# Optimization experiments

Measured on AMD Instinct MI355X. Metric: run time of the kernel, lower is better.

Reference implementation:

```python
import jax, jax.numpy as jnp
import numpy as np

N = 100000   # nodes (single node type 'A')
C = 256      # hidden_channels
OUT = 128    # out_channels
E_RAND = 300000  # random edges; total E = N + E_RAND = 400000
LN_EPS = 1e-5


def _linear_params(key, in_c, out_c):
    kw, kb = jax.random.split(key)
    bound = 1.0 / np.sqrt(in_c)
    W = jax.random.uniform(kw, (out_c, in_c), minval=-bound, maxval=bound, dtype=jnp.float32)
    b = jax.random.uniform(kb, (out_c,), minval=-bound, maxval=bound, dtype=jnp.float32)
    return W, b


def _edges(key):
    # guarantee every node appears in both rows -> unique()/remap in the torch
    # code is the identity, so the subgraph equals the full graph
    k0, k1 = jax.random.split(key)
    base = jnp.arange(N, dtype=jnp.int64)
    row0 = jnp.concatenate([base, jax.random.randint(k0, (E_RAND,), 0, N, dtype=jnp.int64)])
    row1 = jnp.concatenate([base, jax.random.randint(k1, (E_RAND,), 0, N, dtype=jnp.int64)])
    return jnp.stack([row0, row1])


def setup_inputs() -> dict:
    key = jax.random.key(0)
    ks = jax.random.split(key, 12)
    x = jax.random.normal(ks[0], (N, C), dtype=jnp.float32)
    edge_index_r0 = _edges(ks[1])
    edge_index_r1 = _edges(ks[2])
    wl0, bl0 = _linear_params(ks[3], C, C)
    w00, b00 = _linear_params(ks[4], C, C)
    w10, b10 = _linear_params(ks[5], C, C)
    wl1, bl1 = _linear_params(ks[6], C, C)
    w01, b01 = _linear_params(ks[7], C, C)
    w11, b11 = _linear_params(ks[8], C, C)
    Wout, bout = _linear_params(ks[9], C, OUT)
    return dict(
        x=x, edge_index_r0=edge_index_r0, edge_index_r1=edge_index_r1,
        wl0=wl0, bl0=bl0, w00=w00, b00=b00, w10=w10, b10=b10,
        gate0=jnp.float32(0.5), lns0=jnp.ones((C,), jnp.float32), lnb0=jnp.zeros((C,), jnp.float32),
        wl1=wl1, bl1=bl1, w01=w01, b01=b01, w11=w11, b11=b11,
        gate1=jnp.float32(0.5), lns1=jnp.ones((C,), jnp.float32), lnb1=jnp.zeros((C,), jnp.float32),
        Wout=Wout, bout=bout,
    )


def _metapath_layer(x0, h, ei, wl, bl, w0, b0, w1, b1, gate, lns, lnb):
    n = h.shape[0]
    src, dst = ei[0], ei[1]
    # PyG flow='target_to_source', aggr='add': message x_j = h[edge_index[1]],
    # scatter-added at edge_index[0]
    agg = jax.ops.segment_sum(h[dst], src, num_segments=n)
    # original code normalizes by bincount of edge_index[1] (kept faithfully)
    deg = jax.ops.segment_sum(jnp.ones_like(dst, dtype=h.dtype), dst, num_segments=n)
    agg = agg / jnp.clip(deg, 1.0)[:, None]
    g = jax.nn.sigmoid(gate)
    out = (agg @ wl.T + bl) + (1.0 - g) * (h @ w0.T + b0) + g * (x0 @ w1.T + b1)
    out = jax.nn.relu(out)
    mu = out.mean(-1, keepdims=True)
    var = out.var(-1, keepdims=True)
    out = (out - mu) / jnp.sqrt(var + LN_EPS) * lns + lnb
    return out  # dropout is identity in eval mode


def reference(x, edge_index_r0, edge_index_r1,
              wl0, bl0, w00, b00, w10, b10, gate0, lns0, lnb0,
              wl1, bl1, w01, b01, w11, b11, gate1, lns1, lnb1,
              Wout, bout):
    x0 = jax.lax.stop_gradient(x)  # x0_dict is detached in the torch code
    h = x
    # metapath is processed in reverse: conv index 1 first, then conv index 0
    h = _metapath_layer(x0, h, edge_index_r1, wl1, bl1, w01, b01, w11, b11, gate1, lns1, lnb1)
    h = _metapath_layer(x0, h, edge_index_r0, wl0, bl0, w00, b00, w10, b10, gate0, lns0, lnb0)
    return h @ Wout.T + bout
```

## Files before the change

kernel.cpp:

```cpp
#include <hip/hip_runtime.h>

typedef unsigned short u16;
typedef unsigned int   u32;

typedef __attribute__((ext_vector_type(8))) __bf16 bf16x8;
typedef __attribute__((ext_vector_type(8))) unsigned short u16x8;
typedef __attribute__((ext_vector_type(4))) float  f32x4;

#define C      256
#define OUTC   128
#define LN_EPS 1e-5f

__device__ __forceinline__ float bf2f(u16 u) {
    u32 i = ((u32)u) << 16; float f; __builtin_memcpy(&f, &i, 4); return f;
}
__device__ __forceinline__ u16 f2bf(float f) {
    u32 i; __builtin_memcpy(&i, &f, 4);
    u32 r = (i + 0x7FFFu + ((i >> 16) & 1u)) >> 16;
    return (u16)r;
}
__device__ __forceinline__ void load_lds16(const void* g, void* l) {
    __builtin_amdgcn_global_load_lds((const __attribute__((address_space(1))) u32*)g,
                                     (__attribute__((address_space(3))) u32*)l, 16, 0, 0);
}
__device__ __forceinline__ int swz(int row) { return (row + (row >> 2)) & 3; }

#define PREP_BLK 1408
__global__ void prep_combo(const float* wl0, const float* w00, const float* w10,
                           const float* bl0, const float* b00, const float* b10,
                           const float* gate0,
                           const float* wl1, const float* w01, const float* w11,
                           const float* bl1, const float* b01, const float* b11,
                           const float* gate1,
                           const float* Wout, const float* x,
                           u16* __restrict__ WcatA, u16* __restrict__ WcatB,
                           u16* __restrict__ Woutb, float* __restrict__ bcat,
                           u16* __restrict__ xb, size_t n8)
{
    if (blockIdx.x >= PREP_BLK) {
        size_t i = ((size_t)(blockIdx.x - PREP_BLK) * 256 + threadIdx.x);
        if (i >= n8) return;
        const float* p = x + i * 8;
        float4 v0 = *(const float4*)p;
        float4 v1 = *(const float4*)(p + 4);
        u16x8 o;
        o[0] = f2bf(v0.x); o[1] = f2bf(v0.y); o[2] = f2bf(v0.z); o[3] = f2bf(v0.w);
        o[4] = f2bf(v1.x); o[5] = f2bf(v1.y); o[6] = f2bf(v1.z); o[7] = f2bf(v1.w);
        *(u16x8*)(xb + i * 8) = o;
        return;
    }
    int idx = blockIdx.x * 256 + threadIdx.x;
    float gA = 1.f / (1.f + expf(-gate1[0]));
    float gB = 1.f / (1.f + expf(-gate0[0]));
    if (idx < 256 * 512) {
        int n = idx >> 9, k = idx & 511;
        float v;
        if (k < 256) v = wl1[n * 256 + k];
        else         v = (1.f - gA) * w01[n * 256 + (k - 256)] + gA * w11[n * 256 + (k - 256)];
        WcatA[idx] = f2bf(v);
    } else if (idx < 256 * 512 + 256 * 768) {
        int j = idx - 256 * 512;
        int n = j / 768, k = j - n * 768;
        float v;
        if (k < 256)      v = wl0[n * 256 + k];
        else if (k < 512) v = (1.f - gB) * w00[n * 256 + (k - 256)];
        else              v = gB * w10[n * 256 + (k - 512)];
        WcatB[j] = f2bf(v);
    } else {
        int j = idx - (256 * 512 + 256 * 768);
        if (j < OUTC * C) Woutb[j] = f2bf(Wout[j]);
    }
    if (idx < 512) {
        int nn = idx & 255;
        if (idx < 256) bcat[idx] = bl1[nn] + (1.f - gA) * b01[nn] + gA * b11[nn];
        else           bcat[idx] = bl0[nn] + (1.f - gB) * b00[nn] + gB * b10[nn];
    }
}

__global__ void count_edges2(const int* __restrict__ ei1, const int* __restrict__ ei0,
                             int* __restrict__ cnt1, int* __restrict__ deg1,
                             int* __restrict__ cnt0, int* __restrict__ deg0,
                             int E, int Nn, int ebg)
{
    int b = blockIdx.x;
    const int* ei; int *cnt, *deg;
    if (b < ebg) { ei = ei1; cnt = cnt1; deg = deg1; }
    else         { b -= ebg; ei = ei0; cnt = cnt0; deg = deg0; }
    int idx = b * 256 + threadIdx.x;
    if (idx >= E) return;
    int s = ei[idx], d = ei[E + idx];
    if ((unsigned)s >= (unsigned)Nn || (unsigned)d >= (unsigned)Nn) return;
    atomicAdd(cnt + s, 1);
    atomicAdd(deg + d, 1);
}

__global__ void block_sums2(const int* __restrict__ cnt1, const int* __restrict__ cnt0,
                            int* __restrict__ parts1, int* __restrict__ parts0,
                            int n, int nblk)
{
    int b = blockIdx.x;
    const int* counts; int* partials;
    if (b < nblk) { counts = cnt1; partials = parts1; }
    else          { b -= nblk; counts = cnt0; partials = parts0; }
    int i = b * 256 + threadIdx.x;
    int v = (i < n) ? counts[i] : 0;
    #pragma unroll
    for (int off = 32; off; off >>= 1) v += __shfl_down(v, off, 64);
    __shared__ int ws[4];
    if ((threadIdx.x & 63) == 0) ws[threadIdx.x >> 6] = v;
    __syncthreads();
    if (threadIdx.x == 0) partials[b] = ws[0] + ws[1] + ws[2] + ws[3];
}

__global__ void scan_partials2(int* __restrict__ parts1, int* __restrict__ parts0, int nblk)
{
    int* partials = blockIdx.x ? parts0 : parts1;
    __shared__ int buf[1024];
    int tid = threadIdx.x;
    int v = (tid < nblk) ? partials[tid] : 0;
    buf[tid] = v; __syncthreads();
    for (int off = 1; off < 1024; off <<= 1) {
        int t = (tid >= off) ? buf[tid - off] : 0;
        __syncthreads();
        buf[tid] += t;
        __syncthreads();
    }
    if (tid < nblk) partials[tid] = buf[tid] - v;
}

__global__ void make_offsets2(int* __restrict__ cnt1, int* __restrict__ cnt0,
                              const int* __restrict__ parts1, const int* __restrict__ parts0,
                              int* __restrict__ off1a, int* __restrict__ off0a,
                              int n, int nblk)
{
    int b = blockIdx.x;
    int* counts_cursor; const int* partials; int* offsets;
    if (b < nblk) { counts_cursor = cnt1; partials = parts1; offsets = off1a; }
    else          { b -= nblk; counts_cursor = cnt0; partials = parts0; offsets = off0a; }
    __shared__ int buf[256];
    int i = b * 256 + threadIdx.x;
    int cnt = (i < n) ? counts_cursor[i] : 0;
    buf[threadIdx.x] = cnt; __syncthreads();
    for (int off = 1; off < 256; off <<= 1) {
        int t = (threadIdx.x >= off) ? buf[threadIdx.x - off] : 0;
        __syncthreads();
        buf[threadIdx.x] += t;
        __syncthreads();
    }
    int off = partials[b] + buf[threadIdx.x] - cnt;
    if (i < n) {
        offsets[i] = off;
        counts_cursor[i] = off;
        if (i == n - 1) offsets[n] = off + cnt;
    }
}

__global__ void fill_edges2(const int* __restrict__ ei1, const int* __restrict__ ei0,
                            int* __restrict__ cur1, int* __restrict__ cur0,
                            int* __restrict__ ed1, int* __restrict__ ed0,
                            int E, int Nn, int ebg)
{
    int b = blockIdx.x;
    const int* ei; int *cursor, *edgedst;
    if (b < ebg) { ei = ei1; cursor = cur1; edgedst = ed1; }
    else         { b -= ebg; ei = ei0; cursor = cur0; edgedst = ed0; }
    int idx = b * 256 + threadIdx.x;
    if (idx >= E) return;
    int s = ei[idx], d = ei[E + idx];
    if ((unsigned)s >= (unsigned)Nn || (unsigned)d >= (unsigned)Nn) return;
    int p = atomicAdd(cursor + s, 1);
    edgedst[p] = d;
}

__global__ __launch_bounds__(256) void gather_kernel(
    const int* __restrict__ offsets, const int* __restrict__ edgedst,
    const int* __restrict__ degcnt, const u16* __restrict__ h,
    u16* __restrict__ aggb, int Nn)
{
    int node = blockIdx.x * 4 + (threadIdx.x >> 6);
    if (node >= Nn) return;
    int lane = threadIdx.x & 63;
    int beg = offsets[node], end = offsets[node + 1];
    float4 a0 = {0.f, 0.f, 0.f, 0.f}, a1 = {0.f, 0.f, 0.f, 0.f};
    int e = beg;
    for (; e + 1 < end; e += 2) {
        int d0 = edgedst[e], d1 = edgedst[e + 1];
        ushort4 v0 = *(const ushort4*)(h + (size_t)d0 * C + lane * 4);
        ushort4 v1 = *(const ushort4*)(h + (size_t)d1 * C + lane * 4);
        a0.x += bf2f(v0.x); a0.y += bf2f(v0.y); a0.z += bf2f(v0.z); a0.w += bf2f(v0.w);
        a1.x += bf2f(v1.x); a1.y += bf2f(v1.y); a1.z += bf2f(v1.z); a1.w += bf2f(v1.w);
    }
    if (e < end) {
        int d0 = edgedst[e];
        ushort4 v0 = *(const ushort4*)(h + (size_t)d0 * C + lane * 4);
        a0.x += bf2f(v0.x); a0.y += bf2f(v0.y); a0.z += bf2f(v0.z); a0.w += bf2f(v0.w);
    }
    float inv = 1.0f / fmaxf((float)degcnt[node], 1.0f);
    ushort4 o;
    o.x = f2bf((a0.x + a1.x) * inv); o.y = f2bf((a0.y + a1.y) * inv);
    o.z = f2bf((a0.z + a1.z) * inv); o.w = f2bf((a0.w + a1.w) * inv);
    *(ushort4*)(aggb + (size_t)node * C + lane * 4) = o;
}

template <int NSEG>
__global__ __launch_bounds__(512, 4) void layer_gemm(
    const u16* __restrict__ s0, const u16* __restrict__ s1, const u16* __restrict__ s2,
    const u16* __restrict__ W,
    const float* __restrict__ bcat,
    const float* __restrict__ lns, const float* __restrict__ lnb,
    u16* __restrict__ Hout, int Nnodes)
{
    constexpr int WK = NSEG * 256;
    constexpr int KT = NSEG * 8;

    __shared__ u16 Alds[2][128 * 32];
    __shared__ u16 Blds[2][256 * 32];
    __shared__ float lnpart[128][4][2];

    const int tid  = threadIdx.x;
    const int wave = tid >> 6, lane = tid & 63;
    const int wave_m = wave & 1, wave_n = wave >> 1;
    const int q = lane >> 4, l15 = lane & 15;
    const int m0 = blockIdx.x * 128;

    const int srow = (wave << 4) + (lane >> 2);
    int anode = m0 + srow; if (anode >= Nnodes) anode = Nnodes - 1;
    const int asc = (lane & 3) ^ swz(srow);
    const size_t a_goff = (size_t)anode * C + asc * 8;
    const int a_lo = wave << 9;

    const u16* bgp[2]; int b_lo[2];
    #pragma unroll
    for (int i = 0; i < 2; ++i) {
        int cb = wave + i * 8;
        int brow = (cb << 4) + (lane >> 2);
        int bsc = (lane & 3) ^ swz(brow);
        bgp[i]  = W + brow * WK + bsc * 8;
        b_lo[i] = cb << 9;
    }

    int aoff[4], boff[4];
    #pragma unroll
    for (int t = 0; t < 4; ++t) {
        int ar = wave_m * 64 + t * 16 + l15;
        aoff[t] = ar * 32 + ((q ^ swz(ar)) << 3);
        int br = wave_n * 64 + t * 16 + l15;
        boff[t] = br * 32 + ((q ^ swz(br)) << 3);
    }

    f32x4 acc[4][4] = {};

    auto stage = [&](int b, int kt) {
        const u16* Asrc = (kt < 8) ? s0 : ((NSEG == 2 || kt < 16) ? s1 : s2);
        load_lds16(Asrc + a_goff + ((kt & 7) << 5), &Alds[b][a_lo]);
        int k0 = kt << 5;
        load_lds16(bgp[0] + k0, &Blds[b][b_lo[0]]);
        load_lds16(bgp[1] + k0, &Blds[b][b_lo[1]]);
    };
    auto compute = [&](const u16* __restrict__ Ab, const u16* __restrict__ Bb) {
        bf16x8 af[4], bfr[4];
        #pragma unroll
        for (int t = 0; t < 4; ++t) af[t]  = *(const bf16x8*)(Ab + aoff[t]);
        #pragma unroll
        for (int f = 0; f < 4; ++f) bfr[f] = *(const bf16x8*)(Bb + boff[f]);
        #pragma unroll
        for (int t = 0; t < 4; ++t)
            #pragma unroll
            for (int f = 0; f < 4; ++f)
                acc[t][f] = __builtin_amdgcn_mfma_f32_16x16x32_bf16(af[t], bfr[f], acc[t][f], 0, 0, 0);
    };

    stage(0, 0);
    stage(1, 1);
    for (int kt = 0; kt < KT - 2; kt += 2) {
        asm volatile("s_waitcnt vmcnt(3)" ::: "memory");
        __builtin_amdgcn_s_barrier();
        __builtin_amdgcn_sched_barrier(0);
        compute(&Alds[0][0], &Blds[0][0]);
        __builtin_amdgcn_sched_barrier(0);
        __builtin_amdgcn_s_barrier();
        stage(0, kt + 2);
        asm volatile("s_waitcnt vmcnt(3)" ::: "memory");
        __builtin_amdgcn_s_barrier();
        __builtin_amdgcn_sched_barrier(0);
        compute(&Alds[1][0], &Blds[1][0]);
        __builtin_amdgcn_sched_barrier(0);
        __builtin_amdgcn_s_barrier();
        stage(1, kt + 3);
    }
    asm volatile("s_waitcnt vmcnt(3)" ::: "memory");
    __builtin_amdgcn_s_barrier();
    __builtin_amdgcn_sched_barrier(0);
    compute(&Alds[0][0], &Blds[0][0]);
    asm volatile("s_waitcnt vmcnt(0)" ::: "memory");
    __builtin_amdgcn_s_barrier();
    __builtin_amdgcn_sched_barrier(0);
    compute(&Alds[1][0], &Blds[1][0]);

    float bias[4], lsc[4], lbi[4];
    #pragma unroll
    for (int f = 0; f < 4; ++f) {
        int n = wave_n * 64 + f * 16 + l15;
        bias[f] = bcat[n]; lsc[f] = lns[n]; lbi[f] = lnb[n];
    }
    #pragma unroll
    for (int t = 0; t < 4; ++t)
        #pragma unroll
        for (int r = 0; r < 4; ++r) {
            float p = 0.f, pp = 0.f;
            #pragma unroll
            for (int f = 0; f < 4; ++f) {
                float v = acc[t][f][r] + bias[f];
                v = fmaxf(v, 0.f);
                acc[t][f][r] = v;
                p += v; pp += v * v;
            }
            #pragma unroll
            for (int off = 1; off < 16; off <<= 1) {
                p  += __shfl_xor(p,  off, 16);
                pp += __shfl_xor(pp, off, 16);
            }
            if (l15 == 0) {
                int row = wave_m * 64 + t * 16 + q * 4 + r;
                lnpart[row][wave_n][0] = p;
                lnpart[row][wave_n][1] = pp;
            }
        }
    __syncthreads();
    #pragma unroll
    for (int t = 0; t < 4; ++t)
        #pragma unroll
        for (int r = 0; r < 4; ++r) {
            int row = wave_m * 64 + t * 16 + q * 4 + r;
            int node = m0 + row;
            if (node < Nnodes) {
                float S1 = lnpart[row][0][0] + lnpart[row][1][0]
                         + lnpart[row][2][0] + lnpart[row][3][0];
                float S2 = lnpart[row][0][1] + lnpart[row][1][1]
                         + lnpart[row][2][1] + lnpart[row][3][1];
                float mean = S1 * (1.f / 256.f);
                float var  = fmaxf(S2 * (1.f / 256.f) - mean * mean, 0.f);
                float rstd = rsqrtf(var + LN_EPS);
                u16* op = Hout + (size_t)node * C;
                #pragma unroll
                for (int f = 0; f < 4; ++f) {
                    int n = wave_n * 64 + f * 16 + l15;
                    op[n] = f2bf((acc[t][f][r] - mean) * rstd * lsc[f] + lbi[f]);
                }
            }
        }
}

__global__ __launch_bounds__(512, 4) void final_gemm(
    const u16* __restrict__ A, const u16* __restrict__ W,
    const float* __restrict__ bout, float* __restrict__ out, int Nnodes)
{
    __shared__ u16 Alds[2][128 * 32];
    __shared__ u16 Blds[2][128 * 32];

    const int tid = threadIdx.x;
    const int wave = tid >> 6, lane = tid & 63;
    const int wave_m = wave & 1, wave_n = wave >> 1;
    const int q = lane >> 4, l15 = lane & 15;
    const int m0 = blockIdx.x * 128;

    const int srow = (wave << 4) + (lane >> 2);
    int anode = m0 + srow; if (anode >= Nnodes) anode = Nnodes - 1;
    const int asc = (lane & 3) ^ swz(srow);
    const size_t a_goff = (size_t)anode * C + asc * 8;
    const int a_lo = wave << 9;

    const int bsc = (lane & 3) ^ swz(srow);
    const u16* bgp = W + srow * C + bsc * 8;
    const int b_lo = wave << 9;

    int aoff[4], boff[2];
    #pragma unroll
    for (int t = 0; t < 4; ++t) {
        int ar = wave_m * 64 + t * 16 + l15;
        aoff[t] = ar * 32 + ((q ^ swz(ar)) << 3);
    }
    #pragma unroll
    for (int f = 0; f < 2; ++f) {
        int br = wave_n * 32 + f * 16 + l15;
        boff[f] = br * 32 + ((q ^ swz(br)) << 3);
    }

    f32x4 acc[4][2] = {};

    auto stage = [&](int b, int kt) {
        int k0 = kt << 5;
        load_lds16(A + a_goff + k0, &Alds[b][a_lo]);
        load_lds16(bgp + k0, &Blds[b][b_lo]);
    };
    auto compute = [&](const u16* __restrict__ Ab, const u16* __restrict__ Bb) {
        bf16x8 af[4], bfr[2];
        #pragma unroll
        for (int t = 0; t < 4; ++t) af[t]  = *(const bf16x8*)(Ab + aoff[t]);
        #pragma unroll
        for (int f = 0; f < 2; ++f) bfr[f] = *(const bf16x8*)(Bb + boff[f]);
        #pragma unroll
        for (int t = 0; t < 4; ++t)
            #pragma unroll
            for (int f = 0; f < 2; ++f)
                acc[t][f] = __builtin_amdgcn_mfma_f32_16x16x32_bf16(af[t], bfr[f], acc[t][f], 0, 0, 0);
    };

    stage(0, 0);
    stage(1, 1);
    for (int kt = 0; kt < 6; kt += 2) {
        asm volatile("s_waitcnt vmcnt(2)" ::: "memory");
        __builtin_amdgcn_s_barrier();
        __builtin_amdgcn_sched_barrier(0);
        compute(&Alds[0][0], &Blds[0][0]);
        __builtin_amdgcn_sched_barrier(0);
        __builtin_amdgcn_s_barrier();
        stage(0, kt + 2);
        asm volatile("s_waitcnt vmcnt(2)" ::: "memory");
        __builtin_amdgcn_s_barrier();
        __builtin_amdgcn_sched_barrier(0);
        compute(&Alds[1][0], &Blds[1][0]);
        __builtin_amdgcn_sched_barrier(0);
        __builtin_amdgcn_s_barrier();
        stage(1, kt + 3);
    }
    asm volatile("s_waitcnt vmcnt(2)" ::: "memory");
    __builtin_amdgcn_s_barrier();
    __builtin_amdgcn_sched_barrier(0);
    compute(&Alds[0][0], &Blds[0][0]);
    asm volatile("s_waitcnt vmcnt(0)" ::: "memory");
    __builtin_amdgcn_s_barrier();
    __builtin_amdgcn_sched_barrier(0);
    compute(&Alds[1][0], &Blds[1][0]);

    float bias[2];
    #pragma unroll
    for (int f = 0; f < 2; ++f) bias[f] = bout[wave_n * 32 + f * 16 + l15];
    #pragma unroll
    for (int t = 0; t < 4; ++t)
        #pragma unroll
        for (int r = 0; r < 4; ++r) {
            int row = wave_m * 64 + t * 16 + q * 4 + r;
            int node = m0 + row;
            if (node < Nnodes) {
                float* op = out + (size_t)node * OUTC;
                #pragma unroll
                for (int f = 0; f < 2; ++f) {
                    int n = wave_n * 32 + f * 16 + l15;
                    op[n] = acc[t][f][r] + bias[f];
                }
            }
        }
}

extern "C" void kernel_launch(void* const* d_in, const int* in_sizes, int n_in,
                              void* d_out, int out_size, void* d_ws, size_t ws_size,
                              hipStream_t stream)
{
    const float* x    = (const float*)d_in[0];
    const int*   ei0  = (const int*)d_in[1];
    const int*   ei1  = (const int*)d_in[2];
    const float* wl0  = (const float*)d_in[3];
    const float* bl0  = (const float*)d_in[4];
    const float* w00  = (const float*)d_in[5];
    const float* b00  = (const float*)d_in[6];
    const float* w10  = (const float*)d_in[7];
    const float* b10  = (const float*)d_in[8];
    const float* gate0= (const float*)d_in[9];
    const float* lns0 = (const float*)d_in[10];
    const float* lnb0 = (const float*)d_in[11];
    const float* wl1  = (const float*)d_in[12];
    const float* bl1  = (const float*)d_in[13];
    const float* w01  = (const float*)d_in[14];
    const float* b01  = (const float*)d_in[15];
    const float* w11  = (const float*)d_in[16];
    const float* b11  = (const float*)d_in[17];
    const float* gate1= (const float*)d_in[18];
    const float* lns1 = (const float*)d_in[19];
    const float* lnb1 = (const float*)d_in[20];
    const float* Wout = (const float*)d_in[21];
    const float* bout = (const float*)d_in[22];

    const int N = in_sizes[0] / C;
    const int E = in_sizes[1] / 2;

    char* w = (char*)d_ws;
    u16*   WcatA = (u16*)w;   w += (size_t)256 * 512 * 2;
    u16*   WcatB = (u16*)w;   w += (size_t)256 * 768 * 2;
    u16*   Woutb = (u16*)w;   w += (size_t)OUTC * C * 2;
    float* bcat  = (float*)w; w += 4096;
    int*   cnt1  = (int*)w;   w += (size_t)N * 4;
    int*   deg1  = (int*)w;   w += (size_t)N * 4;
    int*   cnt0  = (int*)w;   w += (size_t)N * 4;
    int*   deg0  = (int*)w;   w += (size_t)N * 4;
    int*   off1  = (int*)w;   w += (((size_t)(N + 1) * 4) + 255) & ~255ull;
    int*   off0  = (int*)w;   w += (((size_t)(N + 1) * 4) + 255) & ~255ull;
    int*   parts1= (int*)w;   w += 4096;
    int*   parts0= (int*)w;   w += 4096;
    int*   ed1   = (int*)w;   w += (size_t)E * 4;
    int*   ed0   = (int*)w;   w += (size_t)E * 4;
    u16*   xb    = (u16*)w;   w += (size_t)N * C * 2;
    u16*   aggb  = (u16*)w;   w += (size_t)N * C * 2;
    u16*   h1    = (u16*)w;   w += (size_t)N * C * 2;

    const int eb_grid = (E + 255) / 256;
    const int nblk    = (N + 255) / 256;
    const int gt_grid = (N + 3) / 4;
    const int gm_grid = (N + 127) / 128;
    const size_t n8   = (size_t)N * C / 8;
    const int xc_blk  = (int)((n8 + 255) / 256);
    u16* h2 = (u16*)d_out;

    hipMemsetAsync(cnt1, 0, (size_t)4 * N * 4, stream);
    prep_combo<<<PREP_BLK + xc_blk, 256, 0, stream>>>(
        wl0, w00, w10, bl0, b00, b10, gate0,
        wl1, w01, w11, bl1, b01, b11, gate1,
        Wout, x, WcatA, WcatB, Woutb, bcat, xb, n8);

    count_edges2 <<<2 * eb_grid, 256, 0, stream>>>(ei1, ei0, cnt1, deg1, cnt0, deg0, E, N, eb_grid);
    block_sums2  <<<2 * nblk, 256, 0, stream>>>(cnt1, cnt0, parts1, parts0, N, nblk);
    scan_partials2<<<2, 1024, 0, stream>>>(parts1, parts0, nblk);
    make_offsets2<<<2 * nblk, 256, 0, stream>>>(cnt1, cnt0, parts1, parts0, off1, off0, N, nblk);
    fill_edges2  <<<2 * eb_grid, 256, 0, stream>>>(ei1, ei0, cnt1, cnt0, ed1, ed0, E, N, eb_grid);

    gather_kernel<<<gt_grid, 256, 0, stream>>>(off1, ed1, deg1, xb, aggb, N);
    layer_gemm<2><<<gm_grid, 512, 0, stream>>>(aggb, xb, nullptr, WcatA, bcat,
                                               lns1, lnb1, h1, N);

    gather_kernel<<<gt_grid, 256, 0, stream>>>(off0, ed0, deg0, h1, aggb, N);
    layer_gemm<3><<<gm_grid, 512, 0, stream>>>(aggb, h1, xb, WcatB, bcat + C,
                                               lns0, lnb0, h2, N);

    final_gemm<<<gm_grid, 512, 0, stream>>>(h2, Woutb, bout, (float*)d_out, N);
}
```

Baseline: 536.6 us.

## Widen layer GEMM to 256-row tiles with K=64 stages and vectorize gather

The layer GEMM now processes 256 node rows per block instead of 128. It stages 64-wide K slices in two halves using a new swizzled LDS layout held in 136 KB of dynamic shared memory, and interleaves MFMA issue with LDS reads and prefetches under s_setprio. The aim is to double reuse of the concatenated weight tile per block and to hide more global-load latency. The cost is a larger accumulator array, a launch-bounds minimum of 2 blocks instead of 4, and heavy LDS use that limits occupancy. The gather kernel also changes: each half-wave reads 16-byte bf16 vectors for a different edge, and the two halves are combined with a lane shuffle, which means fewer, wider loads per edge row.

```diff
diff --git a/kernel.cpp b/kernel.cpp
--- a/kernel.cpp
+++ b/kernel.cpp
@@ -180,30 +180,45 @@
     int node = blockIdx.x * 4 + (threadIdx.x >> 6);
     if (node >= Nn) return;
     int lane = threadIdx.x & 63;
+    int half = lane >> 5, l5 = lane & 31;
     int beg = offsets[node], end = offsets[node + 1];
-    float4 a0 = {0.f, 0.f, 0.f, 0.f}, a1 = {0.f, 0.f, 0.f, 0.f};
-    int e = beg;
-    for (; e + 1 < end; e += 2) {
-        int d0 = edgedst[e], d1 = edgedst[e + 1];
-        ushort4 v0 = *(const ushort4*)(h + (size_t)d0 * C + lane * 4);
-        ushort4 v1 = *(const ushort4*)(h + (size_t)d1 * C + lane * 4);
-        a0.x += bf2f(v0.x); a0.y += bf2f(v0.y); a0.z += bf2f(v0.z); a0.w += bf2f(v0.w);
-        a1.x += bf2f(v1.x); a1.y += bf2f(v1.y); a1.z += bf2f(v1.z); a1.w += bf2f(v1.w);
-    }
-    if (e < end) {
-        int d0 = edgedst[e];
-        ushort4 v0 = *(const ushort4*)(h + (size_t)d0 * C + lane * 4);
-        a0.x += bf2f(v0.x); a0.y += bf2f(v0.y); a0.z += bf2f(v0.z); a0.w += bf2f(v0.w);
+    float a0[8] = {}, a1[8] = {};
+    int p = beg;
+    for (; p + 3 < end; p += 4) {
+        int d0 = edgedst[p + half];
+        int d1 = edgedst[p + 2 + half];
+        u16x8 v0 = *(const u16x8*)(h + (size_t)d0 * C + l5 * 8);
+        u16x8 v1 = *(const u16x8*)(h + (size_t)d1 * C + l5 * 8);
+        #pragma unroll
+        for (int j = 0; j < 8; ++j) { a0[j] += bf2f(v0[j]); a1[j] += bf2f(v1[j]); }
+    }
+    if (p + 1 < end) {
+        int d0 = edgedst[p + half];
+        u16x8 v0 = *(const u16x8*)(h + (size_t)d0 * C + l5 * 8);
+        #pragma unroll
+        for (int j = 0; j < 8; ++j) a0[j] += bf2f(v0[j]);
+        p += 2;
+    }
+    if (p < end && half == 0) {
+        int d0 = edgedst[p];
+        u16x8 v0 = *(const u16x8*)(h + (size_t)d0 * C + l5 * 8);
+        #pragma unroll
+        for (int j = 0; j < 8; ++j) a1[j] += bf2f(v0[j]);
     }
     float inv = 1.0f / fmaxf((float)degcnt[node], 1.0f);
-    ushort4 o;
-    o.x = f2bf((a0.x + a1.x) * inv); o.y = f2bf((a0.y + a1.y) * inv);
-    o.z = f2bf((a0.z + a1.z) * inv); o.w = f2bf((a0.w + a1.w) * inv);
-    *(ushort4*)(aggb + (size_t)node * C + lane * 4) = o;
+    u16x8 o;
+    #pragma unroll
+    for (int j = 0; j < 8; ++j) {
+        float s = a0[j] + a1[j];
+        s += __shfl_xor(s, 32);
+        o[j] = f2bf(s * inv);
+    }
+    if (half == 0)
+        *(u16x8*)(aggb + (size_t)node * C + l5 * 8) = o;
 }
 
 template <int NSEG>
-__global__ __launch_bounds__(512, 4) void layer_gemm(
+__global__ __launch_bounds__(512, 2) void layer_gemm8(
     const u16* __restrict__ s0, const u16* __restrict__ s1, const u16* __restrict__ s2,
     const u16* __restrict__ W,
     const float* __restrict__ bcat,
@@ -211,91 +226,148 @@
     u16* __restrict__ Hout, int Nnodes)
 {
     constexpr int WK = NSEG * 256;
-    constexpr int KT = NSEG * 8;
-
-    __shared__ u16 Alds[2][128 * 32];
-    __shared__ u16 Blds[2][256 * 32];
-    __shared__ float lnpart[128][4][2];
+    constexpr int T  = NSEG * 4;
+
+    extern __shared__ char smem[];
+    u16*   A_e    = (u16*)smem;
+    u16*   B_e    = (u16*)(smem + 65536);
+    float* lnpart = (float*)(smem + 131072);
 
     const int tid  = threadIdx.x;
     const int wave = tid >> 6, lane = tid & 63;
     const int wave_m = wave & 1, wave_n = wave >> 1;
     const int q = lane >> 4, l15 = lane & 15;
-    const int m0 = blockIdx.x * 128;
-
-    const int srow = (wave << 4) + (lane >> 2);
-    int anode = m0 + srow; if (anode >= Nnodes) anode = Nnodes - 1;
-    const int asc = (lane & 3) ^ swz(srow);
-    const size_t a_goff = (size_t)anode * C + asc * 8;
-    const int a_lo = wave << 9;
-
-    const u16* bgp[2]; int b_lo[2];
+    const int m0 = blockIdx.x * 256;
+
+    size_t a_goff[2], b_goff[2];
+    int ldso[2];
     #pragma unroll
     for (int i = 0; i < 2; ++i) {
-        int cb = wave + i * 8;
-        int brow = (cb << 4) + (lane >> 2);
-        int bsc = (lane & 3) ^ swz(brow);
-        bgp[i]  = W + brow * WK + bsc * 8;
-        b_lo[i] = cb << 9;
-    }
-
-    int aoff[4], boff[4];
-    #pragma unroll
-    for (int t = 0; t < 4; ++t) {
-        int ar = wave_m * 64 + t * 16 + l15;
-        aoff[t] = ar * 32 + ((q ^ swz(ar)) << 3);
-        int br = wave_n * 64 + t * 16 + l15;
-        boff[t] = br * 32 + ((q ^ swz(br)) << 3);
-    }
-
-    f32x4 acc[4][4] = {};
-
-    auto stage = [&](int b, int kt) {
-        const u16* Asrc = (kt < 8) ? s0 : ((NSEG == 2 || kt < 16) ? s1 : s2);
-        load_lds16(Asrc + a_goff + ((kt & 7) << 5), &Alds[b][a_lo]);
-        int k0 = kt << 5;
-        load_lds16(bgp[0] + k0, &Blds[b][b_lo[0]]);
-        load_lds16(bgp[1] + k0, &Blds[b][b_lo[1]]);
+        int o = i * 8192 + wave * 1024 + lane * 16;
+        int g = o >> 7, slot = (o >> 4) & 7;
+        int bc = slot ^ (g & 7);
+        int r = 2 * g + (bc >> 2), c = bc & 3;
+        int node = m0 + r; if (node >= Nnodes) node = Nnodes - 1;
+        a_goff[i] = (size_t)node * C + c * 8;
+        b_goff[i] = (size_t)r * WK + c * 8;
+        ldso[i]   = i * 8192 + wave * 1024;
+    }
+
+    int aoffE[8], boffE[4];
+    #pragma unroll
+    for (int j = 0; j < 8; ++j) {
+        int r = wave_m * 128 + j * 16 + l15;
+        aoffE[j] = (r >> 1) * 64 + (((((r & 1) << 2) | q) ^ ((r >> 1) & 7)) << 3);
+    }
+    #pragma unroll
+    for (int f = 0; f < 4; ++f) {
+        int r = wave_n * 64 + f * 16 + l15;
+        boffE[f] = (r >> 1) * 64 + (((((r & 1) << 2) | q) ^ ((r >> 1) & 7)) << 3);
+    }
+
+    f32x4 acc[8][4] = {};
+
+    auto stA = [&](int buf, int kh, int t) {
+        const u16* sp = (t < 4) ? s0 : ((NSEG == 2 || t < 8) ? s1 : s2);
+        const u16* base = sp + ((t & 3) << 6) + (kh << 5);
+        #pragma unroll
+        for (int i = 0; i < 2; ++i)
+            load_lds16(base + a_goff[i], (char*)A_e + buf * 32768 + kh * 16384 + ldso[i]);
     };
-    auto compute = [&](const u16* __restrict__ Ab, const u16* __restrict__ Bb) {
+    auto stB = [&](int buf, int kh, int t) {
+        const u16* base = W + (t << 6) + (kh << 5);
+        #pragma unroll
+        for (int i = 0; i < 2; ++i)
+            load_lds16(base + b_goff[i], (char*)B_e + buf * 32768 + kh * 16384 + ldso[i]);
+    };
+
+#define LDA(DST, BASE, MH) \
+    _Pragma("unroll") for (int j = 0; j < 4; ++j) \
+        DST[j] = *(const bf16x8*)((BASE) + aoffE[(MH) * 4 + j]);
+#define LDB(DST, BASE) \
+    _Pragma("unroll") for (int f = 0; f < 4; ++f) \
+        DST[f] = *(const bf16x8*)((BASE) + boffE[f]);
+#define MFMA16(MH, AF, BF) \
+    _Pragma("unroll") for (int j = 0; j < 4; ++j) \
+        _Pragma("unroll") for (int f = 0; f < 4; ++f) \
+            acc[(MH) * 4 + j][f] = __builtin_amdgcn_mfma_f32_16x16x32_bf16( \
+                AF[j], BF[f], acc[(MH) * 4 + j][f], 0, 0, 0);
+#define SBAR()  asm volatile("s_barrier" ::: "memory")
+
+    stA(0, 0, 0); stB(0, 0, 0); stA(0, 1, 0); stB(0, 1, 0);
+
+    int cur = 0;
+    for (int t = 0; t < T - 1; ++t, cur ^= 1) {
+        const u16* Ac = A_e + cur * 16384;
+        const u16* Bc = B_e + cur * 16384;
+        const int nxt = cur ^ 1;
         bf16x8 af[4], bfr[4];
-        #pragma unroll
-        for (int t = 0; t < 4; ++t) af[t]  = *(const bf16x8*)(Ab + aoff[t]);
-        #pragma unroll
-        for (int f = 0; f < 4; ++f) bfr[f] = *(const bf16x8*)(Bb + boff[f]);
-        #pragma unroll
-        for (int t = 0; t < 4; ++t)
-            #pragma unroll
-            for (int f = 0; f < 4; ++f)
-                acc[t][f] = __builtin_amdgcn_mfma_f32_16x16x32_bf16(af[t], bfr[f], acc[t][f], 0, 0, 0);
-    };
-
-    stage(0, 0);
-    stage(1, 1);
-    for (int kt = 0; kt < KT - 2; kt += 2) {
-        asm volatile("s_waitcnt vmcnt(3)" ::: "memory");
-        __builtin_amdgcn_s_barrier();
-        __builtin_amdgcn_sched_barrier(0);
-        compute(&Alds[0][0], &Blds[0][0]);
-        __builtin_amdgcn_sched_barrier(0);
-        __builtin_amdgcn_s_barrier();
-        stage(0, kt + 2);
-        asm volatile("s_waitcnt vmcnt(3)" ::: "memory");
-        __builtin_amdgcn_s_barrier();
-        __builtin_amdgcn_sched_barrier(0);
-        compute(&Alds[1][0], &Blds[1][0]);
-        __builtin_amdgcn_sched_barrier(0);
-        __builtin_amdgcn_s_barrier();
-        stage(1, kt + 3);
-    }
-    asm volatile("s_waitcnt vmcnt(3)" ::: "memory");
-    __builtin_amdgcn_s_barrier();
-    __builtin_amdgcn_sched_barrier(0);
-    compute(&Alds[0][0], &Blds[0][0]);
-    asm volatile("s_waitcnt vmcnt(0)" ::: "memory");
-    __builtin_amdgcn_s_barrier();
-    __builtin_amdgcn_sched_barrier(0);
-    compute(&Alds[1][0], &Blds[1][0]);
+        stA(nxt, 0, t + 1);
+        asm volatile("s_waitcnt vmcnt(6)" ::: "memory");
+        SBAR();
+        __builtin_amdgcn_sched_barrier(0);
+        LDB(bfr, Bc); LDA(af, Ac, 0);
+        __builtin_amdgcn_s_setprio(1);
+        MFMA16(0, af, bfr);
+        __builtin_amdgcn_s_setprio(0);
+        SBAR();
+        LDA(af, Ac, 1);
+        stB(nxt, 0, t + 1);
+        SBAR();
+        __builtin_amdgcn_s_setprio(1);
+        MFMA16(1, af, bfr);
+        __builtin_amdgcn_s_setprio(0);
+        SBAR();
+        stA(nxt, 1, t + 1);
+        asm volatile("s_waitcnt vmcnt(6)" ::: "memory");
+        SBAR();
+        __builtin_amdgcn_sched_barrier(0);
+        LDB(bfr, Bc + 8192); LDA(af, Ac + 8192, 0);
+        __builtin_amdgcn_s_setprio(1);
+        MFMA16(0, af, bfr);
+        __builtin_amdgcn_s_setprio(0);
+        SBAR();
+        LDA(af, Ac + 8192, 1);
+        stB(nxt, 1, t + 1);
+        SBAR();
+        __builtin_amdgcn_s_setprio(1);
+        MFMA16(1, af, bfr);
+        __builtin_amdgcn_s_setprio(0);
+        SBAR();
+    }
+    {
+        const u16* Ac = A_e + cur * 16384;
+        const u16* Bc = B_e + cur * 16384;
+        bf16x8 af[4], bfr[4];
+        asm volatile("s_waitcnt vmcnt(4)" ::: "memory");
+        SBAR();
+        __builtin_amdgcn_sched_barrier(0);
+        LDB(bfr, Bc); LDA(af, Ac, 0);
+        __builtin_amdgcn_s_setprio(1);
+        MFMA16(0, af, bfr);
+        __builtin_amdgcn_s_setprio(0);
+        SBAR();
+        LDA(af, Ac, 1);
+        SBAR();
+        __builtin_amdgcn_s_setprio(1);
+        MFMA16(1, af, bfr);
+        __builtin_amdgcn_s_setprio(0);
+        SBAR();
+        asm volatile("s_waitcnt vmcnt(0)" ::: "memory");
+        SBAR();
+        __builtin_amdgcn_sched_barrier(0);
+        LDB(bfr, Bc + 8192); LDA(af, Ac + 8192, 0);
+        __builtin_amdgcn_s_setprio(1);
+        MFMA16(0, af, bfr);
+        __builtin_amdgcn_s_setprio(0);
+        SBAR();
+        LDA(af, Ac + 8192, 1);
+        SBAR();
+        __builtin_amdgcn_s_setprio(1);
+        MFMA16(1, af, bfr);
+        __builtin_amdgcn_s_setprio(0);
+        SBAR();
+    }
 
     float bias[4], lsc[4], lbi[4];
     #pragma unroll
@@ -304,15 +376,15 @@
         bias[f] = bcat[n]; lsc[f] = lns[n]; lbi[f] = lnb[n];
     }
     #pragma unroll
-    for (int t = 0; t < 4; ++t)
+    for (int t8 = 0; t8 < 8; ++t8)
         #pragma unroll
         for (int r = 0; r < 4; ++r) {
             float p = 0.f, pp = 0.f;
             #pragma unroll
             for (int f = 0; f < 4; ++f) {
-                float v = acc[t][f][r] + bias[f];
+                float v = acc[t8][f][r] + bias[f];
                 v = fmaxf(v, 0.f);
-                acc[t][f][r] = v;
+                acc[t8][f][r] = v;
                 p += v; pp += v * v;
             }
             #pragma unroll
@@ -321,23 +393,23 @@
                 pp += __shfl_xor(pp, off, 16);
             }
             if (l15 == 0) {
-                int row = wave_m * 64 + t * 16 + q * 4 + r;
-                lnpart[row][wave_n][0] = p;
-                lnpart[row][wave_n][1] = pp;
+                int row = wave_m * 128 + t8 * 16 + q * 4 + r;
+                lnpart[row * 8 + wave_n * 2 + 0] = p;
+                lnpart[row * 8 + wave_n * 2 + 1] = pp;
             }
         }
     __syncthreads();
     #pragma unroll
-    for (int t = 0; t < 4; ++t)
+    for (int t8 = 0; t8 < 8; ++t8)
         #pragma unroll
         for (int r = 0; r < 4; ++r) {
-            int row = wave_m * 64 + t * 16 + q * 4 + r;
+            int row = wave_m * 128 + t8 * 16 + q * 4 + r;
             int node = m0 + row;
             if (node < Nnodes) {
-                float S1 = lnpart[row][0][0] + lnpart[row][1][0]
-                         + lnpart[row][2][0] + lnpart[row][3][0];
-                float S2 = lnpart[row][0][1] + lnpart[row][1][1]
-                         + lnpart[row][2][1] + lnpart[row][3][1];
+                float S1 = lnpart[row * 8 + 0] + lnpart[row * 8 + 2]
+                         + lnpart[row * 8 + 4] + lnpart[row * 8 + 6];
+                float S2 = lnpart[row * 8 + 1] + lnpart[row * 8 + 3]
+                         + lnpart[row * 8 + 5] + lnpart[row * 8 + 7];
                 float mean = S1 * (1.f / 256.f);
                 float var  = fmaxf(S2 * (1.f / 256.f) - mean * mean, 0.f);
                 float rstd = rsqrtf(var + LN_EPS);
@@ -345,10 +417,14 @@
                 #pragma unroll
                 for (int f = 0; f < 4; ++f) {
                     int n = wave_n * 64 + f * 16 + l15;
-                    op[n] = f2bf((acc[t][f][r] - mean) * rstd * lsc[f] + lbi[f]);
+                    op[n] = f2bf((acc[t8][f][r] - mean) * rstd * lsc[f] + lbi[f]);
                 }
             }
         }
+#undef LDA
+#undef LDB
+#undef MFMA16
+#undef SBAR
 }
 
 __global__ __launch_bounds__(512, 4) void final_gemm(
@@ -507,8 +583,10 @@
     const int nblk    = (N + 255) / 256;
     const int gt_grid = (N + 3) / 4;
     const int gm_grid = (N + 127) / 128;
+    const int gm8     = (N + 255) / 256;
     const size_t n8   = (size_t)N * C / 8;
     const int xc_blk  = (int)((n8 + 255) / 256);
+    const size_t lds8 = 139264;
     u16* h2 = (u16*)d_out;
 
     hipMemsetAsync(cnt1, 0, (size_t)4 * N * 4, stream);
@@ -524,11 +602,11 @@
     fill_edges2  <<<2 * eb_grid, 256, 0, stream>>>(ei1, ei0, cnt1, cnt0, ed1, ed0, E, N, eb_grid);
 
     gather_kernel<<<gt_grid, 256, 0, stream>>>(off1, ed1, deg1, xb, aggb, N);
-    layer_gemm<2><<<gm_grid, 512, 0, stream>>>(aggb, xb, nullptr, WcatA, bcat,
+    layer_gemm8<2><<<gm8, 512, lds8, stream>>>(aggb, xb, nullptr, WcatA, bcat,
                                                lns1, lnb1, h1, N);
 
     gather_kernel<<<gt_grid, 256, 0, stream>>>(off0, ed0, deg0, h1, aggb, N);
-    layer_gemm<3><<<gm_grid, 512, 0, stream>>>(aggb, h1, xb, WcatB, bcat + C,
+    layer_gemm8<3><<<gm8, 512, lds8, stream>>>(aggb, h1, xb, WcatB, bcat + C,
                                                lns0, lnb0, h2, N);
 
     final_gemm<<<gm_grid, 512, 0, stream>>>(h2, Woutb, bout, (float*)d_out, N);
```

Result: no change. 541.0 us (+0.8%).
